# Performance work log

Measured on AMD Instinct MI355X. Metric: run time of the kernel, lower is better.

## Reference

```python
import jax, jax.numpy as jnp
import numpy as np

N_NODES, N_EDGES, C_IN = 50000, 320000, 512
DIMS = [C_IN, 2048, 1024, 512, 256, 128]


def setup_inputs() -> dict:
    key = jax.random.key(0)
    ks = jax.random.split(key, 2 + 2 * 5)
    inp = {
        "x": jax.random.normal(ks[0], (N_NODES, C_IN), jnp.float32),
        "edge_index": jax.random.randint(ks[1], (2, N_EDGES), 0, N_NODES, dtype=jnp.int64),
    }
    for i in range(5):
        fan_in = DIMS[i]
        inp[f"W{i+1}"] = jax.random.normal(ks[2 + 2 * i], (DIMS[i], DIMS[i + 1]), jnp.float32) / np.float32(np.sqrt(fan_in))
        inp[f"b{i+1}"] = jnp.zeros((DIMS[i + 1],), jnp.float32)
    return inp


def _gcn_layer(h, W, b, src, dst, dinv, n_nodes):
    # PyG GCNConv: h' = D^{-1/2} (A + I) D^{-1/2} (h W) + b, deg includes self-loop
    h = h @ W                                  # [N, out]
    norm = (dinv[src] * dinv[dst])[:, None]    # per-edge normalization
    agg = jax.ops.segment_sum(h[src] * norm, dst, num_segments=n_nodes)
    agg = agg + h * (dinv * dinv)[:, None]     # self-loop contribution
    return agg + b


def reference(x, edge_index, W1, b1, W2, b2, W3, b3, W4, b4, W5, b5):
    n = x.shape[0]
    src, dst = edge_index[0], edge_index[1]
    # in-degree (at dst) + 1 for self-loop, as in PyG gcn_norm
    deg = jax.ops.segment_sum(jnp.ones(src.shape[0], x.dtype), dst, num_segments=n) + 1.0
    dinv = jax.lax.rsqrt(deg)
    # dropout is identity in eval mode (training=False)
    h = jax.nn.relu(_gcn_layer(x, W1, b1, src, dst, dinv, n))
    h = jax.nn.relu(_gcn_layer(h, W2, b2, src, dst, dinv, n))
    h = jax.nn.relu(_gcn_layer(h, W3, b3, src, dst, dinv, n))
    h = jax.nn.relu(_gcn_layer(h, W4, b4, src, dst, dinv, n))
    return _gcn_layer(h, W5, b5, src, dst, dinv, n)
```

## Files before the change

### kernel.cpp

```cpp
#include <hip/hip_runtime.h>
#include <hip/hip_bf16.h>
#include <stdint.h>

#define N_NODES 50000
#define N_EDGES 320000
#define MP 50048

typedef __hip_bfloat16 bf16_t;
typedef __attribute__((ext_vector_type(8))) short short8;
typedef __attribute__((ext_vector_type(4))) float floatx4;

__global__ void detect_kernel(const int* __restrict__ ei, int* __restrict__ flag) {
    int tid = threadIdx.x;
    int v = ei[2 * tid + 1];
    unsigned long long b = __ballot(v != 0);
    if (tid == 0) *flag = (b == 0ull) ? 1 : 0;
}

__device__ __forceinline__ int load_edge(const int* ei, int row, int e, int is64) {
    long pos = (long)row * N_EDGES + e;
    return is64 ? ei[2 * pos] : ei[pos];
}

__global__ void count_kernel(const int* __restrict__ ei, const int* __restrict__ flag,
                             int* __restrict__ counts) {
    int e = blockIdx.x * 256 + threadIdx.x;
    if (e < N_EDGES) {
        int d = load_edge(ei, 1, e, *flag);
        atomicAdd(&counts[d], 1);
    }
}

__global__ __launch_bounds__(1024)
void scan_kernel(const int* __restrict__ counts, int* __restrict__ rowptr,
                 int* __restrict__ cursor, float* __restrict__ dinv,
                 float* __restrict__ selfw) {
    __shared__ int wsum[16];
    __shared__ int base_s;
    int tid  = threadIdx.x;
    int lane = tid & 63;
    int wv   = tid >> 6;
    if (tid == 0) base_s = 0;
    __syncthreads();
    for (int start = 0; start < N_NODES; start += 1024) {
        int i = start + tid;
        int v = (i < N_NODES) ? counts[i] : 0;
        int s = v;
#pragma unroll
        for (int off = 1; off < 64; off <<= 1) {
            int t = __shfl_up(s, off, 64);
            if (lane >= off) s += t;
        }
        if (lane == 63) wsum[wv] = s;
        __syncthreads();
        if (wv == 0 && lane < 16) {
            int t = wsum[lane];
#pragma unroll
            for (int off = 1; off < 16; off <<= 1) {
                int u = __shfl_up(t, off, 64);
                if (lane >= off) t += u;
            }
            wsum[lane] = t;
        }
        __syncthreads();
        int wbase = (wv == 0) ? 0 : wsum[wv - 1];
        int incl  = s + wbase;
        int base  = base_s;
        if (i < N_NODES) {
            int excl = base + incl - v;
            rowptr[i] = excl;
            cursor[i] = excl;
            float di = rsqrtf((float)v + 1.0f);
            dinv[i] = di;
            selfw[i] = di * di;
        }
        __syncthreads();
        if (tid == 1023) base_s = base + incl;
        __syncthreads();
    }
    if (tid == 0) rowptr[N_NODES] = N_EDGES;
}

__global__ void fill_kernel(const int* __restrict__ ei, const int* __restrict__ flag,
                            int* __restrict__ cursor, const float* __restrict__ dinv,
                            int* __restrict__ esrc, float* __restrict__ ewt) {
    int e = blockIdx.x * 256 + threadIdx.x;
    if (e < N_EDGES) {
        int is64 = *flag;
        int s = load_edge(ei, 0, e, is64);
        int d = load_edge(ei, 1, e, is64);
        int p = atomicAdd(&cursor[d], 1);
        esrc[p] = s;
        ewt[p]  = dinv[s] * dinv[d];
    }
}

__global__ void cast_x_kernel(const float* __restrict__ x, bf16_t* __restrict__ xb) {
    long idx = ((long)blockIdx.x * 256 + threadIdx.x) * 4;
    if (idx >= (long)MP * 512) return;
    union { bf16_t h[4]; uint2 u; } o;
    long row = idx >> 9;
    if (row < N_NODES) {
        float4 v = *(const float4*)(x + idx);
        o.h[0] = __float2bfloat16(v.x);
        o.h[1] = __float2bfloat16(v.y);
        o.h[2] = __float2bfloat16(v.z);
        o.h[3] = __float2bfloat16(v.w);
    } else {
        o.u = make_uint2(0u, 0u);
    }
    *(uint2*)(xb + idx) = o.u;
}

__global__ void cast_w_kernel(const float* __restrict__ W, bf16_t* __restrict__ Wt,
                              int K, int Nn) {
    int idx = blockIdx.x * 256 + threadIdx.x;
    if (idx >= K * Nn) return;
    int n = idx % Nn;
    int k = idx / Nn;
    Wt[(size_t)n * K + k] = __float2bfloat16(W[idx]);
}

#define BM 128
#define BN 128
#define BK 64

__device__ __forceinline__ void stage16(const bf16_t* g, bf16_t* l) {
    __builtin_amdgcn_global_load_lds(
        (const __attribute__((address_space(1))) void*)g,
        (__attribute__((address_space(3))) void*)l, 16, 0, 0);
}

__global__ __launch_bounds__(256)
void gemm_bf16(const bf16_t* __restrict__ A, const bf16_t* __restrict__ Bt,
               bf16_t* __restrict__ C, int K, int Nn,
               const float* __restrict__ bias, int relu, int nx, int ny) {
    int id   = blockIdx.x;
    int xcd  = id & 7;
    int slot = id >> 3;
    int y    = (slot / nx) * 8 + xcd;
    int xt   = slot % nx;
    if (y >= ny) return;

    __shared__ __align__(16) bf16_t ldsA[BM * BK];
    __shared__ __align__(16) bf16_t ldsB[BN * BK];

    int tid  = threadIdx.x;
    int lane = tid & 63;
    int wave = tid >> 6;
    int m15  = lane & 15;
    int quad = lane >> 4;
    int wm = (wave & 1) * 64;
    int wn = (wave >> 1) * 64;
    long bm0 = (long)y * BM;
    long bn0 = (long)xt * BN;

    floatx4 acc[4][4] = {};

    int rb   = tid >> 3;
    int cole = ((tid & 7) ^ (rb & 7)) * 8;
    const bf16_t* pa = A  + (bm0 + rb) * (long)K + cole;
    const bf16_t* pb = Bt + (bn0 + rb) * (long)K + cole;
    bf16_t* la = ldsA + tid * 8;
    bf16_t* lb = ldsB + tid * 8;
    const long step32 = 32 * (long)K;

    int fx   = lane & 7;
    int blk0 = ((0 + quad) ^ fx) * 8;
    int blk1 = ((4 + quad) ^ fx) * 8;
    int rowA = (wm + m15) * BK;
    int rowB = (wn + m15) * BK;

    for (int k0 = 0; k0 < K; k0 += BK) {
#pragma unroll
        for (int it = 0; it < 4; ++it) {
            stage16(pa + it * step32, la + it * 2048);
            stage16(pb + it * step32, lb + it * 2048);
        }
        pa += BK;
        pb += BK;
        __syncthreads();
#pragma unroll
        for (int kk = 0; kk < 2; ++kk) {
            int blk = kk ? blk1 : blk0;
            short8 af[4], bfr[4];
#pragma unroll
            for (int i = 0; i < 4; ++i)
                af[i] = *(const short8*)(&ldsA[rowA + i * (16 * BK) + blk]);
#pragma unroll
            for (int j = 0; j < 4; ++j)
                bfr[j] = *(const short8*)(&ldsB[rowB + j * (16 * BK) + blk]);
#pragma unroll
            for (int i = 0; i < 4; ++i)
#pragma unroll
                for (int j = 0; j < 4; ++j)
                    acc[i][j] = __builtin_amdgcn_mfma_f32_16x16x32_bf16(af[i], bfr[j], acc[i][j], 0, 0, 0);
        }
        __syncthreads();
    }

#pragma unroll
    for (int i = 0; i < 4; ++i) {
#pragma unroll
        for (int j = 0; j < 4; ++j) {
            long row0 = bm0 + wm + i * 16 + quad * 4;
            long col  = bn0 + wn + j * 16 + m15;
            float bv = bias ? bias[col] : 0.f;
#pragma unroll
            for (int r = 0; r < 4; ++r) {
                float v = acc[i][j][r] + bv;
                if (relu) v = fmaxf(v, 0.f);
                C[(row0 + r) * (long)Nn + col] = __float2bfloat16(v);
            }
        }
    }
}

__device__ __forceinline__ void unpack8(uint4 v, float* f) {
    uint32_t u[4] = {v.x, v.y, v.z, v.w};
#pragma unroll
    for (int i = 0; i < 4; ++i) {
        f[2 * i]     = __uint_as_float(u[i] << 16);
        f[2 * i + 1] = __uint_as_float(u[i] & 0xffff0000u);
    }
}

__global__ __launch_bounds__(256)
void agg_kernel(const bf16_t* __restrict__ hW, const int* __restrict__ rowptr,
                const int* __restrict__ esrc, const float* __restrict__ ewt,
                const float* __restrict__ selfw,
                const float* __restrict__ bias, bf16_t* __restrict__ outb,
                float* __restrict__ outf, int Nn, int chunks, int relu, int rows) {
    int wave = threadIdx.x >> 6;
    int lane = threadIdx.x & 63;
    long unit = (long)blockIdx.x * 4 + wave;
    if (unit >= (long)rows * chunks) return;
    int n     = (int)(unit / chunks);
    int chunk = (int)(unit % chunks);
    int c0 = chunk * 512 + lane * 8;
    if (c0 >= Nn) return;

    if (n >= N_NODES) {
        if (outb) *(uint4*)(outb + (size_t)n * Nn + c0) = make_uint4(0, 0, 0, 0);
        return;
    }

    int r0 = rowptr[n], r1 = rowptr[n + 1];
    float acc[8] = {};

    int e = r0;
    for (; e + 4 <= r1; e += 4) {
        int s0 = esrc[e], s1 = esrc[e + 1], s2 = esrc[e + 2], s3 = esrc[e + 3];
        float w0 = ewt[e], w1 = ewt[e + 1], w2 = ewt[e + 2], w3 = ewt[e + 3];
        uint4 v0 = *(const uint4*)(hW + (size_t)s0 * Nn + c0);
        uint4 v1 = *(const uint4*)(hW + (size_t)s1 * Nn + c0);
        uint4 v2 = *(const uint4*)(hW + (size_t)s2 * Nn + c0);
        uint4 v3 = *(const uint4*)(hW + (size_t)s3 * Nn + c0);
        float f0[8], f1[8], f2[8], f3[8];
        unpack8(v0, f0); unpack8(v1, f1); unpack8(v2, f2); unpack8(v3, f3);
#pragma unroll
        for (int j = 0; j < 8; ++j)
            acc[j] += f0[j] * w0 + f1[j] * w1 + f2[j] * w2 + f3[j] * w3;
    }
    for (; e < r1; ++e) {
        int s = esrc[e];
        float w = ewt[e];
        uint4 v = *(const uint4*)(hW + (size_t)s * Nn + c0);
        float fv[8]; unpack8(v, fv);
#pragma unroll
        for (int j = 0; j < 8; ++j) acc[j] += fv[j] * w;
    }

    {
        uint4 v = *(const uint4*)(hW + (size_t)n * Nn + c0);
        float fv[8]; unpack8(v, fv);
        float w = selfw[n];
#pragma unroll
        for (int j = 0; j < 8; ++j) acc[j] += fv[j] * w;
    }
    if (bias) {
#pragma unroll
        for (int j = 0; j < 8; ++j) acc[j] += bias[c0 + j];
    }
    if (relu) {
#pragma unroll
        for (int j = 0; j < 8; ++j) acc[j] = fmaxf(acc[j], 0.f);
    }
    if (outf) {
        *(float4*)(outf + (size_t)n * Nn + c0)     = make_float4(acc[0], acc[1], acc[2], acc[3]);
        *(float4*)(outf + (size_t)n * Nn + c0 + 4) = make_float4(acc[4], acc[5], acc[6], acc[7]);
    } else {
        union { bf16_t h[8]; uint4 u; } o;
#pragma unroll
        for (int j = 0; j < 8; ++j) o.h[j] = __float2bfloat16(acc[j]);
        *(uint4*)(outb + (size_t)n * Nn + c0) = o.u;
    }
}

extern "C" void kernel_launch(void* const* d_in, const int* in_sizes, int n_in,
                              void* d_out, int out_size, void* d_ws, size_t ws_size,
                              hipStream_t stream) {
    (void)in_sizes; (void)n_in; (void)out_size; (void)ws_size;
    const float* x  = (const float*)d_in[0];
    const int*   ei = (const int*)d_in[1];
    const float* W[5] = {(const float*)d_in[2], (const float*)d_in[4], (const float*)d_in[6],
                         (const float*)d_in[8], (const float*)d_in[10]};
    const float* B[5] = {(const float*)d_in[3], (const float*)d_in[5], (const float*)d_in[7],
                         (const float*)d_in[9], (const float*)d_in[11]};
    static const int dims[6] = {512, 2048, 1024, 512, 256, 128};

    const size_t SZ_A = (size_t)MP * 512 * 2;
    const size_t SZ_B = (size_t)MP * 512 * 2;
    const size_t SZ_C = (size_t)MP * 2048 * 2;
    char* base = (char*)d_ws;
    bf16_t* regA = (bf16_t*)base;
    bf16_t* regB = (bf16_t*)(base + SZ_A);
    bf16_t* regC = (bf16_t*)(base + SZ_A + SZ_B);
    char* p = base + SZ_A + SZ_B + SZ_C;
    auto take = [&](size_t bytes) { char* r = p; p += (bytes + 255) & ~(size_t)255; return r; };
    bf16_t* wt[5];
    for (int i = 0; i < 5; ++i) wt[i] = (bf16_t*)take((size_t)dims[i] * dims[i + 1] * 2);
    int*   counts = (int*)take((size_t)N_NODES * 4);
    int*   rowptr = (int*)take((size_t)(N_NODES + 1) * 4);
    int*   cursor = (int*)take((size_t)N_NODES * 4);
    int*   esrc   = (int*)take((size_t)N_EDGES * 4);
    float* ewt    = (float*)take((size_t)N_EDGES * 4);
    float* dinv   = (float*)take((size_t)N_NODES * 4);
    float* selfw  = (float*)take((size_t)N_NODES * 4);
    int*   eflag  = (int*)take(256);

    detect_kernel<<<1, 64, 0, stream>>>(ei, eflag);
    hipMemsetAsync(counts, 0, (size_t)N_NODES * 4, stream);
    count_kernel<<<(N_EDGES + 255) / 256, 256, 0, stream>>>(ei, eflag, counts);
    scan_kernel<<<1, 1024, 0, stream>>>(counts, rowptr, cursor, dinv, selfw);
    fill_kernel<<<(N_EDGES + 255) / 256, 256, 0, stream>>>(ei, eflag, cursor, dinv, esrc, ewt);

    bf16_t* xb = regA;
    cast_x_kernel<<<(int)(((long)MP * 512 / 4 + 255) / 256), 256, 0, stream>>>(x, xb);
    for (int i = 0; i < 5; ++i) {
        int kn = dims[i] * dims[i + 1];
        cast_w_kernel<<<(kn + 255) / 256, 256, 0, stream>>>(W[i], wt[i], dims[i], dims[i + 1]);
    }

    auto launch_gemm = [&](const bf16_t* a, const bf16_t* bt, bf16_t* c,
                           int K, int Nn, const float* bias, int relu) {
        int nx = Nn / BN;
        int ny = MP / BM;
        int blocks = nx * (((ny + 7) / 8) * 8);
        gemm_bf16<<<blocks, 256, 0, stream>>>(a, bt, c, K, Nn, bias, relu, nx, ny);
    };

    auto launch_agg = [&](const bf16_t* hw, const float* bias, bf16_t* outb,
                          float* outf, int Nn, int relu, int rows) {
        int chunks = (Nn + 511) / 512;
        long units = (long)rows * chunks;
        int blocks = (int)((units + 3) / 4);
        agg_kernel<<<blocks, 256, 0, stream>>>(hw, rowptr, esrc, ewt, selfw, bias,
                                               outb, outf, Nn, chunks, relu, rows);
    };

    bf16_t* g1 = regB;
    bf16_t* h1 = regC;
    launch_agg(xb, nullptr, g1, nullptr, 512, 0, MP);
    launch_gemm(g1, wt[0], h1, 512, 2048, B[0], 1);

    bf16_t* hwbuf[4] = {regA, regA, regA, regA};
    bf16_t* hbuf[3]  = {regC, regB, regB};
    const bf16_t* hin = h1;
    for (int l = 1; l < 5; ++l) {
        int K = dims[l], Nn = dims[l + 1];
        bf16_t* hw = hwbuf[l - 1];
        launch_gemm(hin, wt[l], hw, K, Nn, nullptr, 0);
        if (l < 4) {
            bf16_t* hn = hbuf[l - 1];
            launch_agg(hw, B[l], hn, nullptr, Nn, 1, MP);
            hin = hn;
        } else {
            launch_agg(hw, B[l], nullptr, (float*)d_out, Nn, 0, N_NODES);
        }
    }
}
```

Baseline: 1.112 ms.

## Fuse preprocessing casts into one kernel and pack multiple nodes per wave in aggregation

Merges the edge-count, x-cast and five weight-cast kernels into a single block-partitioned preprocessing launch, removing several launches. The aggregation kernel now maps several nodes to one wave when the feature width is below 512, so the 256- and 128-wide layers no longer leave most lanes idle. The edge loop handles the tail with clamped, zero-weighted loads instead of a separate remainder loop. Packing different nodes into one wave can cause divergence, since their edge counts differ.

```diff
diff --git a/kernel.cpp b/kernel.cpp
--- a/kernel.cpp
+++ b/kernel.cpp
@@ -22,12 +22,55 @@
     return is64 ? ei[2 * pos] : ei[pos];
 }
 
-__global__ void count_kernel(const int* __restrict__ ei, const int* __restrict__ flag,
-                             int* __restrict__ counts) {
-    int e = blockIdx.x * 256 + threadIdx.x;
-    if (e < N_EDGES) {
-        int d = load_edge(ei, 1, e, *flag);
-        atomicAdd(&counts[d], 1);
+#define CB 1250
+#define XB 25024
+#define WB 14976
+
+__global__ __launch_bounds__(256)
+void preproc_kernel(const int* __restrict__ ei, const int* __restrict__ flag,
+                    int* __restrict__ counts,
+                    const float* __restrict__ x, bf16_t* __restrict__ xb,
+                    const float* __restrict__ W1, const float* __restrict__ W2,
+                    const float* __restrict__ W3, const float* __restrict__ W4,
+                    const float* __restrict__ W5,
+                    bf16_t* __restrict__ wt1, bf16_t* __restrict__ wt2,
+                    bf16_t* __restrict__ wt3, bf16_t* __restrict__ wt4,
+                    bf16_t* __restrict__ wt5) {
+    int bid = blockIdx.x;
+    int tid = threadIdx.x;
+    if (bid < CB) {
+        int e = bid * 256 + tid;
+        if (e < N_EDGES) {
+            int d = load_edge(ei, 1, e, *flag);
+            atomicAdd(&counts[d], 1);
+        }
+    } else if (bid < CB + XB) {
+        long idx = ((long)(bid - CB) * 256 + tid) * 4;
+        union { bf16_t h[4]; uint2 u; } o;
+        long row = idx >> 9;
+        if (row < N_NODES) {
+            float4 v = *(const float4*)(x + idx);
+            o.h[0] = __float2bfloat16(v.x);
+            o.h[1] = __float2bfloat16(v.y);
+            o.h[2] = __float2bfloat16(v.z);
+            o.h[3] = __float2bfloat16(v.w);
+        } else {
+            o.u = make_uint2(0u, 0u);
+        }
+        *(uint2*)(xb + idx) = o.u;
+    } else {
+        long idx = (long)(bid - CB - XB) * 256 + tid;
+        const float* Ws; bf16_t* Wd; int K, Nn; long off;
+        if      (idx < 1048576) { Ws = W1; Wd = wt1; K = 512;  Nn = 2048; off = 0; }
+        else if (idx < 3145728) { Ws = W2; Wd = wt2; K = 2048; Nn = 1024; off = 1048576; }
+        else if (idx < 3670016) { Ws = W3; Wd = wt3; K = 1024; Nn = 512;  off = 3145728; }
+        else if (idx < 3801088) { Ws = W4; Wd = wt4; K = 512;  Nn = 256;  off = 3670016; }
+        else if (idx < 3833856) { Ws = W5; Wd = wt5; K = 256;  Nn = 128;  off = 3801088; }
+        else return;
+        long i = idx - off;
+        int nn = (int)(i & (Nn - 1));
+        int kk = (int)(i >> __builtin_ctz(Nn));
+        Wd[(size_t)nn * K + kk] = __float2bfloat16(Ws[i]);
     }
 }
 
@@ -95,32 +138,6 @@
     }
 }
 
-__global__ void cast_x_kernel(const float* __restrict__ x, bf16_t* __restrict__ xb) {
-    long idx = ((long)blockIdx.x * 256 + threadIdx.x) * 4;
-    if (idx >= (long)MP * 512) return;
-    union { bf16_t h[4]; uint2 u; } o;
-    long row = idx >> 9;
-    if (row < N_NODES) {
-        float4 v = *(const float4*)(x + idx);
-        o.h[0] = __float2bfloat16(v.x);
-        o.h[1] = __float2bfloat16(v.y);
-        o.h[2] = __float2bfloat16(v.z);
-        o.h[3] = __float2bfloat16(v.w);
-    } else {
-        o.u = make_uint2(0u, 0u);
-    }
-    *(uint2*)(xb + idx) = o.u;
-}
-
-__global__ void cast_w_kernel(const float* __restrict__ W, bf16_t* __restrict__ Wt,
-                              int K, int Nn) {
-    int idx = blockIdx.x * 256 + threadIdx.x;
-    if (idx >= K * Nn) return;
-    int n = idx % Nn;
-    int k = idx / Nn;
-    Wt[(size_t)n * K + k] = __float2bfloat16(W[idx]);
-}
-
 #define BM 128
 #define BN 128
 #define BK 64
@@ -230,15 +247,21 @@
                 const int* __restrict__ esrc, const float* __restrict__ ewt,
                 const float* __restrict__ selfw,
                 const float* __restrict__ bias, bf16_t* __restrict__ outb,
-                float* __restrict__ outf, int Nn, int chunks, int relu, int rows) {
+                float* __restrict__ outf, int Nn, int chunks, int npw, int nsh,
+                int relu, int rows) {
     int wave = threadIdx.x >> 6;
     int lane = threadIdx.x & 63;
     long unit = (long)blockIdx.x * 4 + wave;
-    if (unit >= (long)rows * chunks) return;
-    int n     = (int)(unit / chunks);
-    int chunk = (int)(unit % chunks);
-    int c0 = chunk * 512 + lane * 8;
-    if (c0 >= Nn) return;
+    int n, c0;
+    if (npw > 1) {
+        int l8 = lane * 8;
+        n  = (int)(unit * npw + (l8 >> nsh));
+        c0 = l8 & (Nn - 1);
+    } else {
+        n  = (int)(unit / chunks);
+        c0 = (int)(unit % chunks) * 512 + lane * 8;
+    }
+    if (n >= rows || c0 >= Nn) return;
 
     if (n >= N_NODES) {
         if (outb) *(uint4*)(outb + (size_t)n * Nn + c0) = make_uint4(0, 0, 0, 0);
@@ -248,10 +271,15 @@
     int r0 = rowptr[n], r1 = rowptr[n + 1];
     float acc[8] = {};
 
-    int e = r0;
-    for (; e + 4 <= r1; e += 4) {
-        int s0 = esrc[e], s1 = esrc[e + 1], s2 = esrc[e + 2], s3 = esrc[e + 3];
-        float w0 = ewt[e], w1 = ewt[e + 1], w2 = ewt[e + 2], w3 = ewt[e + 3];
+    for (int e = r0; e < r1; e += 4) {
+        int e1 = (e + 1 < r1) ? e + 1 : e;
+        int e2 = (e + 2 < r1) ? e + 2 : e;
+        int e3 = (e + 3 < r1) ? e + 3 : e;
+        int s0 = esrc[e], s1 = esrc[e1], s2 = esrc[e2], s3 = esrc[e3];
+        float w0 = ewt[e];
+        float w1 = (e + 1 < r1) ? ewt[e1] : 0.f;
+        float w2 = (e + 2 < r1) ? ewt[e2] : 0.f;
+        float w3 = (e + 3 < r1) ? ewt[e3] : 0.f;
         uint4 v0 = *(const uint4*)(hW + (size_t)s0 * Nn + c0);
         uint4 v1 = *(const uint4*)(hW + (size_t)s1 * Nn + c0);
         uint4 v2 = *(const uint4*)(hW + (size_t)s2 * Nn + c0);
@@ -261,14 +289,6 @@
 #pragma unroll
         for (int j = 0; j < 8; ++j)
             acc[j] += f0[j] * w0 + f1[j] * w1 + f2[j] * w2 + f3[j] * w3;
-    }
-    for (; e < r1; ++e) {
-        int s = esrc[e];
-        float w = ewt[e];
-        uint4 v = *(const uint4*)(hW + (size_t)s * Nn + c0);
-        float fv[8]; unpack8(v, fv);
-#pragma unroll
-        for (int j = 0; j < 8; ++j) acc[j] += fv[j] * w;
     }
 
     {
@@ -331,16 +351,12 @@
 
     detect_kernel<<<1, 64, 0, stream>>>(ei, eflag);
     hipMemsetAsync(counts, 0, (size_t)N_NODES * 4, stream);
-    count_kernel<<<(N_EDGES + 255) / 256, 256, 0, stream>>>(ei, eflag, counts);
+    bf16_t* xb = regA;
+    preproc_kernel<<<CB + XB + WB, 256, 0, stream>>>(ei, eflag, counts, x, xb,
+                                                     W[0], W[1], W[2], W[3], W[4],
+                                                     wt[0], wt[1], wt[2], wt[3], wt[4]);
     scan_kernel<<<1, 1024, 0, stream>>>(counts, rowptr, cursor, dinv, selfw);
     fill_kernel<<<(N_EDGES + 255) / 256, 256, 0, stream>>>(ei, eflag, cursor, dinv, esrc, ewt);
-
-    bf16_t* xb = regA;
-    cast_x_kernel<<<(int)(((long)MP * 512 / 4 + 255) / 256), 256, 0, stream>>>(x, xb);
-    for (int i = 0; i < 5; ++i) {
-        int kn = dims[i] * dims[i + 1];
-        cast_w_kernel<<<(kn + 255) / 256, 256, 0, stream>>>(W[i], wt[i], dims[i], dims[i + 1]);
-    }
 
     auto launch_gemm = [&](const bf16_t* a, const bf16_t* bt, bf16_t* c,
                            int K, int Nn, const float* bias, int relu) {
@@ -352,11 +368,13 @@
 
     auto launch_agg = [&](const bf16_t* hw, const float* bias, bf16_t* outb,
                           float* outf, int Nn, int relu, int rows) {
-        int chunks = (Nn + 511) / 512;
-        long units = (long)rows * chunks;
+        int chunks = Nn > 512 ? Nn / 512 : 1;
+        int npw    = Nn < 512 ? 512 / Nn : 1;
+        int nsh    = 31 - __builtin_clz(Nn);
+        long units = (long)((rows + npw - 1) / npw) * chunks;
         int blocks = (int)((units + 3) / 4);
         agg_kernel<<<blocks, 256, 0, stream>>>(hw, rowptr, esrc, ewt, selfw, bias,
-                                               outb, outf, Nn, chunks, relu, rows);
+                                               outb, outf, Nn, chunks, npw, nsh, relu, rows);
     };
 
     bf16_t* g1 = regB;
```

After: 1.107 ms. About the same (-0.4%).
